# Optimization experiments

Hardware: AMD Instinct MI355X
Metric: run time of the kernel (lower is better)

## Reference

```python
import jax, jax.numpy as jnp
import numpy as np

B, L, D = 64, 512, 768

def setup_inputs() -> dict:
    key = jax.random.key(0)
    k1, k2, k3, k4 = jax.random.split(key, 4)
    hidden_states = jax.random.normal(k1, (B, L, D), dtype=jnp.float32)
    # nn.Linear(hidden_size, hidden_size): weight [D, D], bias [D]
    W = jax.random.normal(k2, (D, D), dtype=jnp.float32) * (1.0 / np.sqrt(D))
    b = jax.random.normal(k3, (D,), dtype=jnp.float32) * 0.02
    # context_vector: [D, 1]
    context_vector = jax.random.normal(k4, (D, 1), dtype=jnp.float32)
    return {"hidden_states": hidden_states, "W": W, "b": b, "context_vector": context_vector}

def reference(hidden_states, W, b, context_vector):
    # tanh(dense(h)): [B, L, D]; torch Linear uses x @ W.T + b
    proj = jnp.tanh(jnp.einsum('bld,ed->ble', hidden_states, W) + b)
    # scores: [B, L]
    scores = jnp.einsum('bld,d->bl', proj, context_vector[:, 0])
    # softmax over sequence dim (dim=1)
    attention_weights = jax.nn.softmax(scores, axis=1)
    # weighted sum over sequence: [B, D]
    weighted_output = jnp.einsum('bld,bl->bd', hidden_states, attention_weights)
    return (weighted_output, attention_weights)
```

## Files before the change

### kernel.cpp

```cpp
#include <hip/hip_runtime.h>
#include <hip/hip_bf16.h>


using half8 = __attribute__((ext_vector_type(8))) _Float16;
using f32x4 = __attribute__((ext_vector_type(4))) float;

#define AS1 __attribute__((address_space(1)))
#define AS3 __attribute__((address_space(3)))

__device__ __forceinline__ void gload_lds16(const void* g, void* l) {
  __builtin_amdgcn_global_load_lds((const AS1 void*)g, (AS3 void*)l, 16, 0, 0);
}

__device__ __forceinline__ unsigned short f2h(float x) {
  _Float16 h = (_Float16)x;
  return __builtin_bit_cast(unsigned short, h);
}

__device__ __forceinline__ float tanh_fast(float x) {
  return 1.0f - __fdividef(2.0f, 1.0f + __expf(2.0f * x));
}


__global__ void convert_h(const float4* __restrict__ H4, ushort4* __restrict__ Ah) {
  int i = blockIdx.x * 256 + threadIdx.x;
  float4 x = H4[i];
  ushort4 o;
  o.x = f2h(x.x); o.y = f2h(x.y); o.z = f2h(x.z); o.w = f2h(x.w);
  Ah[i] = o;
}

__global__ void convert_w(const float4* __restrict__ W4, ushort4* __restrict__ Wt) {
  int i = blockIdx.x * 256 + threadIdx.x;
  float4 x = W4[i];
  ushort4 o;
  o.x = f2h(x.x); o.y = f2h(x.y); o.z = f2h(x.z); o.w = f2h(x.w);
  Wt[i] = o;
}

__global__ __launch_bounds__(512) void gemm_scores(
    const ushort* __restrict__ Ah, const ushort* __restrict__ Wt,
    const float* __restrict__ bias, const float* __restrict__ cvec,
    float* __restrict__ part) {
  __shared__ ushort ldsA[2][4096];
  __shared__ ushort ldsB[2][24576];
  __shared__ float scpart[4][128];

  const int tid = threadIdx.x;
  const int lane = tid & 63;
  const int wid = tid >> 6;
  const int wr = wid >> 2;
  const int wc = wid & 3;
  const int m = lane & 15, q = lane >> 4;
  const int mtile = blockIdx.x;

  const char* const Abase = (const char*)Ah + (size_t)(mtile * 128) * 1536;
  const char* const Bbase = (const char*)Wt;

  const int alr = tid >> 3;
  const int au = (tid & 7) ^ (alr & 7);
  const size_t asrc = (size_t)(alr + 64 * (au >> 2)) * 1536 + (au & 3) * 16;
  const int bu = (tid & 7) ^ ((tid >> 3) & 7);
  const size_t bsrc0 = (size_t)((tid >> 3) + 384 * (bu >> 2)) * 1536 + (bu & 3) * 16;
  const int wavebase = wid << 10;

  f32x4 acc[4][12];
  #pragma unroll
  for (int i = 0; i < 4; ++i)
    #pragma unroll
    for (int j = 0; j < 12; ++j)
      acc[i][j] = (f32x4){0.f, 0.f, 0.f, 0.f};

  auto stage = [&](int kt, int s) {
    gload_lds16(Abase + asrc + kt * 64, (char*)ldsA[s] + wavebase);
    #pragma unroll
    for (int c = 0; c < 6; ++c)
      gload_lds16(Bbase + bsrc0 + c * 98304 + kt * 64,
                  (char*)ldsB[s] + c * 8192 + wavebase);
  };

  const int aslot = ((wr * 4 + q) ^ (m & 7)) * 16;
  const int bslot = (((wc >> 1) * 4 + q) ^ (m & 7)) * 16;
  const int blr0 = (wc & 1) * 192;

  auto compute = [&](int s) {
    const char* Ab = (const char*)ldsA[s];
    const char* Bb = (const char*)ldsB[s];
    half8 areg[4];
    #pragma unroll
    for (int mi = 0; mi < 4; ++mi)
      areg[mi] = *(const half8*)(Ab + (mi * 16 + m) * 128 + aslot);
    #pragma unroll
    for (int ni = 0; ni < 12; ++ni) {
      half8 breg = *(const half8*)(Bb + (blr0 + ni * 16 + m) * 128 + bslot);
      #pragma unroll
      for (int mi = 0; mi < 4; ++mi)
        acc[mi][ni] = __builtin_amdgcn_mfma_f32_16x16x32_f16(
            areg[mi], breg, acc[mi][ni], 0, 0, 0);
    }
  };

  stage(0, 0);
  __syncthreads();
  #pragma unroll 2
  for (int t = 0; t < 24; ++t) {
    if (t + 1 < 24) stage(t + 1, (t + 1) & 1);
    compute(t & 1);
    __syncthreads();
  }

  float bb[12], cc[12];
  #pragma unroll
  for (int ni = 0; ni < 12; ++ni) {
    int e = wc * 192 + ni * 16 + m;
    bb[ni] = bias[e];
    cc[ni] = cvec[e];
  }
  #pragma unroll
  for (int mi = 0; mi < 4; ++mi) {
    #pragma unroll
    for (int j = 0; j < 4; ++j) {
      float s = 0.f;
      #pragma unroll
      for (int ni = 0; ni < 12; ++ni)
        s += tanh_fast(acc[mi][ni][j] + bb[ni]) * cc[ni];
      s += __shfl_xor(s, 1);
      s += __shfl_xor(s, 2);
      s += __shfl_xor(s, 4);
      s += __shfl_xor(s, 8);
      if (m == 0) scpart[wc][wr * 64 + mi * 16 + q * 4 + j] = s;
    }
  }
  __syncthreads();
  if (tid < 128)
    part[mtile * 128 + tid] =
        scpart[0][tid] + scpart[1][tid] + scpart[2][tid] + scpart[3][tid];
}

__global__ void wsum_fused(const ushort* __restrict__ Ah, const float* __restrict__ prt,
                           float* __restrict__ out) {
  int b = blockIdx.x, dc = blockIdx.y;
  int t = threadIdx.x;
  __shared__ float w[512];
  __shared__ float redm[2], reds[2];

  float s[4];
  #pragma unroll
  for (int i = 0; i < 4; ++i) s[i] = prt[b * 512 + t + i * 128];
  float mx = fmaxf(fmaxf(s[0], s[1]), fmaxf(s[2], s[3]));
  #pragma unroll
  for (int o = 32; o >= 1; o >>= 1) mx = fmaxf(mx, __shfl_xor(mx, o));
  if ((t & 63) == 0) redm[t >> 6] = mx;
  __syncthreads();
  mx = fmaxf(redm[0], redm[1]);

  float e[4], sm = 0.f;
  #pragma unroll
  for (int i = 0; i < 4; ++i) { e[i] = __expf(s[i] - mx); sm += e[i]; }
  #pragma unroll
  for (int o = 32; o >= 1; o >>= 1) sm += __shfl_xor(sm, o);
  if ((t & 63) == 0) reds[t >> 6] = sm;
  __syncthreads();
  float inv = 1.0f / (reds[0] + reds[1]);
  #pragma unroll
  for (int i = 0; i < 4; ++i) w[t + i * 128] = e[i] * inv;
  __syncthreads();

  int d0 = dc * 256 + t * 2;
  const ushort* hp = Ah + (size_t)b * 512 * 768 + d0;
  float a0 = 0.f, a1 = 0.f;
  #pragma unroll 8
  for (int l = 0; l < 512; ++l) {
    unsigned u = *(const unsigned*)(hp + (size_t)l * 768);
    float wl = w[l];
    a0 += wl * (float)__builtin_bit_cast(_Float16, (unsigned short)(u & 0xffff));
    a1 += wl * (float)__builtin_bit_cast(_Float16, (unsigned short)(u >> 16));
  }
  out[b * 768 + d0] = a0;
  out[b * 768 + d0 + 1] = a1;

  if (dc == 0) {
    #pragma unroll
    for (int i = 0; i < 4; ++i)
      out[49152 + b * 512 + t + i * 128] = w[t + i * 128];
  }
}

extern "C" void kernel_launch(void* const* d_in, const int* in_sizes, int n_in,
                              void* d_out, int out_size, void* d_ws, size_t ws_size,
                              hipStream_t stream) {
  const float* H    = (const float*)d_in[0];
  const float* W    = (const float*)d_in[1];
  const float* bias = (const float*)d_in[2];
  const float* cvec = (const float*)d_in[3];
  float* out = (float*)d_out;

  char* ws = (char*)d_ws;
  ushort* Ah = (ushort*)(ws + 0);
  ushort* Wt = (ushort*)(ws + 50331648);
  float*  prt = (float*)(ws + 51511296);

  hipLaunchKernelGGL(convert_h, dim3(24576), dim3(256), 0, stream,
                     (const float4*)H, (ushort4*)Ah);
  hipLaunchKernelGGL(convert_w, dim3(576), dim3(256), 0, stream,
                     (const float4*)W, (ushort4*)Wt);
  hipLaunchKernelGGL(gemm_scores, dim3(256), dim3(512), 0, stream,
                     Ah, Wt, bias, cvec, prt);
  hipLaunchKernelGGL(wsum_fused, dim3(64, 3), dim3(128), 0, stream,
                     Ah, prt, out);
}
```

Before: 114.9 us.

## Retile score GEMM to 256x384 blocks with XCD-aware block mapping

Changes the GEMM block tile from 128 rows by all 768 columns to 256 rows by 384 columns, split into two N-tiles whose partial scores are summed in the softmax kernel. The block-to-tile mapping groups tiles by XCD so that blocks sharing A rows sit on the same chiplet cache. The aim is a more balanced A/B load per block and better L2 reuse. The cost is a second partial-score buffer to read and sum, plus a more complex LDS layout that reuses the operand buffers for the score reduction.

```diff
diff --git a/kernel.cpp b/kernel.cpp
--- a/kernel.cpp
+++ b/kernel.cpp
@@ -42,26 +42,33 @@
     const ushort* __restrict__ Ah, const ushort* __restrict__ Wt,
     const float* __restrict__ bias, const float* __restrict__ cvec,
     float* __restrict__ part) {
-  __shared__ ushort ldsA[2][4096];
-  __shared__ ushort ldsB[2][24576];
-  __shared__ float scpart[4][128];
+  __shared__ ushort ldsAll[40960];
+  ushort* const ldsA0 = ldsAll;
+  ushort* const ldsA1 = ldsAll + 8192;
+  ushort* const ldsB0 = ldsAll + 16384;
+  ushort* const ldsB1 = ldsAll + 28672;
+  float* const scpart = (float*)ldsAll;
 
   const int tid = threadIdx.x;
   const int lane = tid & 63;
   const int wid = tid >> 6;
-  const int wr = wid >> 2;
-  const int wc = wid & 3;
+  const int wr = wid >> 1;
+  const int wc = wid & 1;
   const int m = lane & 15, q = lane >> 4;
-  const int mtile = blockIdx.x;
-
-  const char* const Abase = (const char*)Ah + (size_t)(mtile * 128) * 1536;
-  const char* const Bbase = (const char*)Wt;
-
-  const int alr = tid >> 3;
-  const int au = (tid & 7) ^ (alr & 7);
-  const size_t asrc = (size_t)(alr + 64 * (au >> 2)) * 1536 + (au & 3) * 16;
-  const int bu = (tid & 7) ^ ((tid >> 3) & 7);
-  const size_t bsrc0 = (size_t)((tid >> 3) + 384 * (bu >> 2)) * 1536 + (bu & 3) * 16;
+
+  const int bid = blockIdx.x;
+  const int xcd = bid & 7;
+  const int sid = bid >> 3;
+  const int mtile = xcd * 16 + (sid >> 1);
+  const int ntile = sid & 1;
+
+  const char* const Abase = (const char*)Ah + (size_t)(mtile * 256) * 1536;
+  const char* const Bbase = (const char*)Wt + (size_t)(ntile * 384) * 1536;
+
+  const int up = (tid & 7) ^ ((tid >> 3) & 7);
+  const int tr3 = tid >> 3;
+  const size_t asrc = (size_t)((up >> 2) * 128 + tr3) * 1536 + (up & 3) * 16;
+  const size_t bsrc = (size_t)((up >> 2) * 192 + tr3) * 1536 + (up & 3) * 16;
   const int wavebase = wid << 10;
 
   f32x4 acc[4][12];
@@ -71,28 +78,31 @@
     for (int j = 0; j < 12; ++j)
       acc[i][j] = (f32x4){0.f, 0.f, 0.f, 0.f};
 
-  auto stage = [&](int kt, int s) {
-    gload_lds16(Abase + asrc + kt * 64, (char*)ldsA[s] + wavebase);
-    #pragma unroll
-    for (int c = 0; c < 6; ++c)
-      gload_lds16(Bbase + bsrc0 + c * 98304 + kt * 64,
-                  (char*)ldsB[s] + c * 8192 + wavebase);
+  auto stage = [&](int kt, ushort* dA, ushort* dB) {
+    #pragma unroll
+    for (int c = 0; c < 2; ++c)
+      gload_lds16(Abase + asrc + (size_t)c * 64 * 1536 + kt * 64,
+                  (char*)dA + c * 8192 + wavebase);
+    #pragma unroll
+    for (int c = 0; c < 3; ++c)
+      gload_lds16(Bbase + bsrc + (size_t)c * 64 * 1536 + kt * 64,
+                  (char*)dB + c * 8192 + wavebase);
   };
 
-  const int aslot = ((wr * 4 + q) ^ (m & 7)) * 16;
-  const int bslot = (((wc >> 1) * 4 + q) ^ (m & 7)) * 16;
-  const int blr0 = (wc & 1) * 192;
-
-  auto compute = [&](int s) {
-    const char* Ab = (const char*)ldsA[s];
-    const char* Bb = (const char*)ldsB[s];
+  const int aslot = (((wr >> 1) * 4 + q) ^ (m & 7)) * 16;
+  const int alr0 = (wr & 1) * 64;
+  const int bslot = ((wc * 4 + q) ^ (m & 7)) * 16;
+
+  auto compute = [&](const ushort* As, const ushort* Bs) {
+    const char* Ab = (const char*)As;
+    const char* Bb = (const char*)Bs;
     half8 areg[4];
     #pragma unroll
     for (int mi = 0; mi < 4; ++mi)
-      areg[mi] = *(const half8*)(Ab + (mi * 16 + m) * 128 + aslot);
+      areg[mi] = *(const half8*)(Ab + (alr0 + mi * 16 + m) * 128 + aslot);
     #pragma unroll
     for (int ni = 0; ni < 12; ++ni) {
-      half8 breg = *(const half8*)(Bb + (blr0 + ni * 16 + m) * 128 + bslot);
+      half8 breg = *(const half8*)(Bb + (ni * 16 + m) * 128 + bslot);
       #pragma unroll
       for (int mi = 0; mi < 4; ++mi)
         acc[mi][ni] = __builtin_amdgcn_mfma_f32_16x16x32_f16(
@@ -100,19 +110,23 @@
     }
   };
 
-  stage(0, 0);
+  stage(0, ldsA0, ldsB0);
   __syncthreads();
   #pragma unroll 2
   for (int t = 0; t < 24; ++t) {
-    if (t + 1 < 24) stage(t + 1, (t + 1) & 1);
-    compute(t & 1);
+    ushort* dA = (t & 1) ? ldsA0 : ldsA1;
+    ushort* dB = (t & 1) ? ldsB0 : ldsB1;
+    const ushort* sA = (t & 1) ? ldsA1 : ldsA0;
+    const ushort* sB = (t & 1) ? ldsB1 : ldsB0;
+    if (t + 1 < 24) stage(t + 1, dA, dB);
+    compute(sA, sB);
     __syncthreads();
   }
 
   float bb[12], cc[12];
   #pragma unroll
   for (int ni = 0; ni < 12; ++ni) {
-    int e = wc * 192 + ni * 16 + m;
+    int e = ntile * 384 + wc * 192 + ni * 16 + m;
     bb[ni] = bias[e];
     cc[ni] = cvec[e];
   }
@@ -128,13 +142,12 @@
       s += __shfl_xor(s, 2);
       s += __shfl_xor(s, 4);
       s += __shfl_xor(s, 8);
-      if (m == 0) scpart[wc][wr * 64 + mi * 16 + q * 4 + j] = s;
+      if (m == 0) scpart[wc * 256 + wr * 64 + mi * 16 + q * 4 + j] = s;
     }
   }
   __syncthreads();
-  if (tid < 128)
-    part[mtile * 128 + tid] =
-        scpart[0][tid] + scpart[1][tid] + scpart[2][tid] + scpart[3][tid];
+  if (tid < 256)
+    part[ntile * 32768 + mtile * 256 + tid] = scpart[tid] + scpart[256 + tid];
 }
 
 __global__ void wsum_fused(const ushort* __restrict__ Ah, const float* __restrict__ prt,
@@ -146,7 +159,10 @@
 
   float s[4];
   #pragma unroll
-  for (int i = 0; i < 4; ++i) s[i] = prt[b * 512 + t + i * 128];
+  for (int i = 0; i < 4; ++i) {
+    int r = b * 512 + t + i * 128;
+    s[i] = prt[r] + prt[32768 + r];
+  }
   float mx = fmaxf(fmaxf(s[0], s[1]), fmaxf(s[2], s[3]));
   #pragma unroll
   for (int o = 32; o >= 1; o >>= 1) mx = fmaxf(mx, __shfl_xor(mx, o));
```

Result: faster. 103.1 us (-10.3%).

## Split GEMM N dimension into 128-wide tiles with XCD-aware block mapping

Applied to the files above, without the earlier changes.

The score GEMM now uses 128x128 tiles over 1536 blocks of 256 threads instead of 256 blocks that each covered the full 768-wide N dimension. Block IDs are remapped so the six N tiles of one M tile land on the same XCD and can share A in L2. The main loop is unrolled two stages at a time with fixed LDS buffers. Each N tile writes partial scores to its own slice, and the softmax kernel sums the six partials. This should give better occupancy and fill all CUs, at the cost of reading A six times and extra partial-score traffic.

```diff
diff --git a/kernel.cpp b/kernel.cpp
--- a/kernel.cpp
+++ b/kernel.cpp
@@ -38,81 +38,86 @@
   Wt[i] = o;
 }
 
-__global__ __launch_bounds__(512) void gemm_scores(
+__global__ __launch_bounds__(256) void gemm_scores(
     const ushort* __restrict__ Ah, const ushort* __restrict__ Wt,
     const float* __restrict__ bias, const float* __restrict__ cvec,
     float* __restrict__ part) {
   __shared__ ushort ldsA[2][4096];
-  __shared__ ushort ldsB[2][24576];
-  __shared__ float scpart[4][128];
+  __shared__ ushort ldsB[2][4096];
+  __shared__ float scpart[2][128];
 
   const int tid = threadIdx.x;
   const int lane = tid & 63;
   const int wid = tid >> 6;
-  const int wr = wid >> 2;
-  const int wc = wid & 3;
+  const int wr = wid >> 1, wc = wid & 1;
   const int m = lane & 15, q = lane >> 4;
-  const int mtile = blockIdx.x;
+
+  const int bid = blockIdx.x;
+  const int xcd = bid & 7;
+  const int slot = bid >> 3;
+  const int mtile = xcd * 32 + slot / 6;
+  const int ntile = slot % 6;
 
   const char* const Abase = (const char*)Ah + (size_t)(mtile * 128) * 1536;
-  const char* const Bbase = (const char*)Wt;
-
-  const int alr = tid >> 3;
-  const int au = (tid & 7) ^ (alr & 7);
-  const size_t asrc = (size_t)(alr + 64 * (au >> 2)) * 1536 + (au & 3) * 16;
-  const int bu = (tid & 7) ^ ((tid >> 3) & 7);
-  const size_t bsrc0 = (size_t)((tid >> 3) + 384 * (bu >> 2)) * 1536 + (bu & 3) * 16;
+  const char* const Bbase = (const char*)Wt + (size_t)(ntile * 128) * 1536;
+
+  const int up = (tid & 7) ^ ((tid >> 3) & 7);
+  const int lr_s = tid >> 3;
+  const size_t src0 = (size_t)((up >> 2) * 64 + lr_s) * 1536 + (up & 3) * 16;
+  const size_t src1 = (size_t)((up >> 2) * 64 + 32 + lr_s) * 1536 + (up & 3) * 16;
   const int wavebase = wid << 10;
 
-  f32x4 acc[4][12];
+  f32x4 acc[4][4];
   #pragma unroll
   for (int i = 0; i < 4; ++i)
     #pragma unroll
-    for (int j = 0; j < 12; ++j)
+    for (int j = 0; j < 4; ++j)
       acc[i][j] = (f32x4){0.f, 0.f, 0.f, 0.f};
 
   auto stage = [&](int kt, int s) {
-    gload_lds16(Abase + asrc + kt * 64, (char*)ldsA[s] + wavebase);
-    #pragma unroll
-    for (int c = 0; c < 6; ++c)
-      gload_lds16(Bbase + bsrc0 + c * 98304 + kt * 64,
-                  (char*)ldsB[s] + c * 8192 + wavebase);
+    gload_lds16(Abase + src0 + kt * 64, (char*)ldsA[s] + wavebase);
+    gload_lds16(Abase + src1 + kt * 64, (char*)ldsA[s] + 4096 + wavebase);
+    gload_lds16(Bbase + src0 + kt * 64, (char*)ldsB[s] + wavebase);
+    gload_lds16(Bbase + src1 + kt * 64, (char*)ldsB[s] + 4096 + wavebase);
   };
 
   const int aslot = ((wr * 4 + q) ^ (m & 7)) * 16;
-  const int bslot = (((wc >> 1) * 4 + q) ^ (m & 7)) * 16;
-  const int blr0 = (wc & 1) * 192;
+  const int bslot = ((wc * 4 + q) ^ (m & 7)) * 16;
 
   auto compute = [&](int s) {
     const char* Ab = (const char*)ldsA[s];
     const char* Bb = (const char*)ldsB[s];
-    half8 areg[4];
+    half8 areg[4], breg[4];
     #pragma unroll
     for (int mi = 0; mi < 4; ++mi)
       areg[mi] = *(const half8*)(Ab + (mi * 16 + m) * 128 + aslot);
     #pragma unroll
-    for (int ni = 0; ni < 12; ++ni) {
-      half8 breg = *(const half8*)(Bb + (blr0 + ni * 16 + m) * 128 + bslot);
+    for (int ni = 0; ni < 4; ++ni)
+      breg[ni] = *(const half8*)(Bb + (ni * 16 + m) * 128 + bslot);
+    #pragma unroll
+    for (int mi = 0; mi < 4; ++mi)
       #pragma unroll
-      for (int mi = 0; mi < 4; ++mi)
+      for (int ni = 0; ni < 4; ++ni)
         acc[mi][ni] = __builtin_amdgcn_mfma_f32_16x16x32_f16(
-            areg[mi], breg, acc[mi][ni], 0, 0, 0);
-    }
+            areg[mi], breg[ni], acc[mi][ni], 0, 0, 0);
   };
 
   stage(0, 0);
   __syncthreads();
-  #pragma unroll 2
-  for (int t = 0; t < 24; ++t) {
-    if (t + 1 < 24) stage(t + 1, (t + 1) & 1);
-    compute(t & 1);
+  #pragma unroll
+  for (int kb2 = 0; kb2 < 12; ++kb2) {
+    stage(2 * kb2 + 1, 1);
+    compute(0);
     __syncthreads();
-  }
-
-  float bb[12], cc[12];
-  #pragma unroll
-  for (int ni = 0; ni < 12; ++ni) {
-    int e = wc * 192 + ni * 16 + m;
+    if (kb2 < 11) stage(2 * kb2 + 2, 0);
+    compute(1);
+    __syncthreads();
+  }
+
+  float bb[4], cc[4];
+  #pragma unroll
+  for (int ni = 0; ni < 4; ++ni) {
+    int e = ntile * 128 + wc * 64 + ni * 16 + m;
     bb[ni] = bias[e];
     cc[ni] = cvec[e];
   }
@@ -122,7 +127,7 @@
     for (int j = 0; j < 4; ++j) {
       float s = 0.f;
       #pragma unroll
-      for (int ni = 0; ni < 12; ++ni)
+      for (int ni = 0; ni < 4; ++ni)
         s += tanh_fast(acc[mi][ni][j] + bb[ni]) * cc[ni];
       s += __shfl_xor(s, 1);
       s += __shfl_xor(s, 2);
@@ -133,8 +138,7 @@
   }
   __syncthreads();
   if (tid < 128)
-    part[mtile * 128 + tid] =
-        scpart[0][tid] + scpart[1][tid] + scpart[2][tid] + scpart[3][tid];
+    part[ntile * 32768 + mtile * 128 + tid] = scpart[0][tid] + scpart[1][tid];
 }
 
 __global__ void wsum_fused(const ushort* __restrict__ Ah, const float* __restrict__ prt,
@@ -146,7 +150,11 @@
 
   float s[4];
   #pragma unroll
-  for (int i = 0; i < 4; ++i) s[i] = prt[b * 512 + t + i * 128];
+  for (int i = 0; i < 4; ++i) {
+    int r = b * 512 + t + i * 128;
+    s[i] = prt[r] + prt[32768 + r] + prt[2 * 32768 + r] +
+           prt[3 * 32768 + r] + prt[4 * 32768 + r] + prt[5 * 32768 + r];
+  }
   float mx = fmaxf(fmaxf(s[0], s[1]), fmaxf(s[2], s[3]));
   #pragma unroll
   for (int o = 32; o >= 1; o >>= 1) mx = fmaxf(mx, __shfl_xor(mx, o));
@@ -204,7 +212,7 @@
                      (const float4*)H, (ushort4*)Ah);
   hipLaunchKernelGGL(convert_w, dim3(576), dim3(256), 0, stream,
                      (const float4*)W, (ushort4*)Wt);
-  hipLaunchKernelGGL(gemm_scores, dim3(256), dim3(512), 0, stream,
+  hipLaunchKernelGGL(gemm_scores, dim3(1536), dim3(256), 0, stream,
                      Ah, Wt, bias, cvec, prt);
   hipLaunchKernelGGL(wsum_fused, dim3(64, 3), dim3(128), 0, stream,
                      Ah, prt, out);
```

Result: faster. 112.5 us (-2.1%).
